# Performance work log

Hardware: AMD Instinct MI355X
Metric: run time of the kernel (lower is better)

Reference implementation:

```python
import jax, jax.numpy as jnp
import numpy as np


def cosine_noise_schedule(t):
    # legacy mode: 1 - cos(t/1.008 * pi/2)^2
    return 1.0 - jnp.cos(t / 1.008 * jnp.pi / 2.0) ** 2


def setup_inputs() -> dict:
    key = jax.random.key(0)
    k1, k2, k3 = jax.random.split(key, 3)
    x = jax.random.normal(k1, (256, 3, 32, 32), dtype=jnp.float32)
    images = jax.random.normal(k2, (50000, 3, 32, 32), dtype=jnp.float32)
    t = jax.random.uniform(k3, (1,), dtype=jnp.float32)
    return {"t": t, "x": x, "images": images}


def reference(t, x, images):
    # Exact ideal score: softmax over dataset of Gaussian kernel weights.
    # The original streams dataset batches with an online-softmax running max;
    # with uniform batch sizes that is mathematically a global softmax over N:
    #   score = -(x - at * E_p[y]) / bt^2,  p_j = softmax(-||x - at*y_j||^2 / (2 bt^2))
    sched = cosine_noise_schedule(t)          # [1]
    bt = jnp.sqrt(sched)                      # [1]
    at = jnp.sqrt(1.0 - sched)                # [1]
    b, c, h, w = x.shape
    n = images.shape[0]
    xf = x.reshape(b, -1)                     # [b, chw]
    yf = images.reshape(n, -1)                # [n, chw]
    # ||x - at*y||^2 = ||x||^2 + at^2 ||y||^2 - 2 at x.y  (GEMM-dominant)
    x2 = jnp.sum(xf * xf, axis=1)             # [b]
    y2 = jnp.sum(yf * yf, axis=1)             # [n]
    cross = xf @ yf.T                         # [b, n]
    d2 = x2[:, None] + (at ** 2) * y2[None, :] - 2.0 * at * cross  # [b, n]
    logits = -d2 / (2.0 * bt ** 2)            # [b, n]
    p = jax.nn.softmax(logits, axis=1)        # [b, n], stable (max-subtracted)
    ybar = (p @ yf).reshape(b, c, h, w)       # softmax-weighted dataset mean
    return -(x - at * ybar) / (bt ** 2)
```

## Files before the change

### kernel.cpp

```cpp
#include <hip/hip_runtime.h>

typedef float    f32x4  __attribute__((ext_vector_type(4)));
typedef float    f32x16 __attribute__((ext_vector_type(16)));
typedef _Float16 f16x4  __attribute__((ext_vector_type(4)));
typedef _Float16 f16x8  __attribute__((ext_vector_type(8)));

#define N_IMG 50000
#define NPAD  50176
#define BROWS 256
#define CHW   3072
#define BK    64
#define BM    128
#define BN    128
#define EHS   50176
#define KCHUNK 3136
#define NSPLIT 16

__device__ __forceinline__ void glds16(const void* g, void* l) {
    __builtin_amdgcn_global_load_lds(
        (const __attribute__((address_space(1))) void*)g,
        (__attribute__((address_space(3))) void*)l, 16, 0, 0);
}

__global__ void k_scalars(const float* __restrict__ t, float* __restrict__ sc) {
    if (threadIdx.x == 0) {
        double tv  = (double)t[0];
        double ang = tv * (1.5707963267948966 / 1.008);
        double c   = cos(ang);
        double at  = c;
        double bt2 = 1.0 - c * c;
        sc[0] = (float)at;
        sc[1] = (float)bt2;
        sc[2] = (float)(at / bt2);
        sc[3] = (float)(at * at * 0.5 / bt2);
        sc[4] = (float)(1.0 / bt2);
    }
}

__global__ void k_xprep(const float* __restrict__ x, _Float16* __restrict__ xh) {
    int idx = blockIdx.x * 256 + threadIdx.x;
    f32x4 v = ((const f32x4*)x)[idx];
    f16x4 h;
    h[0] = (_Float16)v[0]; h[1] = (_Float16)v[1];
    h[2] = (_Float16)v[2]; h[3] = (_Float16)v[3];
    ((f16x4*)xh)[idx] = h;
}

__global__ void k_prep(const float* __restrict__ img, _Float16* __restrict__ imgh,
                       float* __restrict__ y2) {
    int row = blockIdx.x, tid = threadIdx.x;
    f16x4* dst = (f16x4*)(imgh + (size_t)row * CHW);
    if (row >= N_IMG) {
        f16x4 z = {(_Float16)0.f, (_Float16)0.f, (_Float16)0.f, (_Float16)0.f};
        #pragma unroll
        for (int i = 0; i < 3; i++) dst[tid + i * 256] = z;
        return;
    }
    const f32x4* src = (const f32x4*)(img + (size_t)row * CHW);
    float s = 0.f;
    #pragma unroll
    for (int i = 0; i < 3; i++) {
        f32x4 v = src[tid + i * 256];
        s += v[0]*v[0] + v[1]*v[1] + v[2]*v[2] + v[3]*v[3];
        f16x4 h;
        h[0] = (_Float16)v[0]; h[1] = (_Float16)v[1];
        h[2] = (_Float16)v[2]; h[3] = (_Float16)v[3];
        dst[tid + i * 256] = h;
    }
    for (int o = 32; o > 0; o >>= 1) s += __shfl_down(s, o);
    __shared__ float wsum[4];
    if ((tid & 63) == 0) wsum[tid >> 6] = s;
    __syncthreads();
    if (tid == 0) y2[row] = (wsum[0] + wsum[1]) + (wsum[2] + wsum[3]);
}

__global__ __launch_bounds__(256, 3) void k_gemm1(
        const _Float16* __restrict__ xh, const _Float16* __restrict__ imgh,
        const float* __restrict__ y2g, const float* __restrict__ sc,
        float* __restrict__ logits) {
    __shared__ _Float16 Alds[BM * BK];
    __shared__ _Float16 Blds[BN * BK];

    const int tid = threadIdx.x;
    const int wid = tid >> 6, lane = tid & 63;
    const int flat = blockIdx.x;
    const int xcd = flat & 7, loc = flat >> 3;
    const int m0 = (loc & 1) * BM;
    const int n0 = (xcd * 49 + (loc >> 1)) * BN;

    const _Float16* gA[4]; const _Float16* gB[4];
    _Float16* lA[4]; _Float16* lB[4];
    #pragma unroll
    for (int j = 0; j < 4; j++) {
        int seg = wid * 4 + j;
        int row = seg * 8 + (lane >> 3);
        int off = (((lane & 7) ^ (row & 7)) << 3);
        gA[j] = xh + (size_t)(m0 + row) * CHW + off;
        int rb = n0 + row; if (rb > N_IMG - 1) rb = N_IMG - 1;
        gB[j] = imgh + (size_t)rb * CHW + off;
        lA[j] = Alds + seg * 512;
        lB[j] = Blds + seg * 512;
    }

    const int wm = wid >> 1, wn = wid & 1;
    const int rm = wm * 64, cn = wn * 64;
    const int lr = lane & 31, hi = lane >> 5;
    const int xm = (lr & 7) << 4;
    const char* Ab = (const char*)Alds;
    const char* Bb = (const char*)Blds;
    const int ar0 = (rm + lr) * 128,      ar1 = (rm + 32 + lr) * 128;
    const int br0 = (cn + lr) * 128,      br1 = (cn + 32 + lr) * 128;
    const int kof = hi * 16;

    f32x16 acc[2][2];
    #pragma unroll
    for (int mi = 0; mi < 2; mi++)
        #pragma unroll
        for (int ni = 0; ni < 2; ni++)
            #pragma unroll
            for (int r = 0; r < 16; r++) acc[mi][ni][r] = 0.f;

    for (int it = 0; it < CHW / BK; ++it) {
        if (it) __syncthreads();
        #pragma unroll
        for (int j = 0; j < 4; j++) glds16(gA[j] + it * BK, lA[j]);
        #pragma unroll
        for (int j = 0; j < 4; j++) glds16(gB[j] + it * BK, lB[j]);
        __syncthreads();
        #pragma unroll
        for (int ks = 0; ks < 4; ++ks) {
            int off = (ks * 32 + kof) ^ xm;
            f16x8 a0 = *(const f16x8*)(Ab + ar0 + off);
            f16x8 a1 = *(const f16x8*)(Ab + ar1 + off);
            f16x8 b0 = *(const f16x8*)(Bb + br0 + off);
            f16x8 b1 = *(const f16x8*)(Bb + br1 + off);
            acc[0][0] = __builtin_amdgcn_mfma_f32_32x32x16_f16(a0, b0, acc[0][0], 0, 0, 0);
            acc[0][1] = __builtin_amdgcn_mfma_f32_32x32x16_f16(a0, b1, acc[0][1], 0, 0, 0);
            acc[1][0] = __builtin_amdgcn_mfma_f32_32x32x16_f16(a1, b0, acc[1][0], 0, 0, 0);
            acc[1][1] = __builtin_amdgcn_mfma_f32_32x32x16_f16(a1, b1, acc[1][1], 0, 0, 0);
        }
    }

    const float c_cross = sc[2], c_y2 = sc[3];
    #pragma unroll
    for (int mi = 0; mi < 2; mi++)
        #pragma unroll
        for (int ni = 0; ni < 2; ni++) {
            int col = n0 + cn + ni * 32 + lr;
            if (col >= N_IMG) continue;
            float y2v = y2g[col];
            f32x16 v = acc[mi][ni];
            #pragma unroll
            for (int r = 0; r < 16; r++) {
                int row = m0 + rm + mi * 32 + (r & 3) + 8 * (r >> 2) + 4 * hi;
                logits[(size_t)row * N_IMG + col] = c_cross * v[r] - c_y2 * y2v;
            }
        }
}

__global__ void k_softmax(const float* __restrict__ logits, _Float16* __restrict__ eh,
                          float* __restrict__ rowsum) {
    int row = blockIdx.x, tid = threadIdx.x;
    const f32x4* lr = (const f32x4*)(logits + (size_t)row * N_IMG);
    _Float16* erow = eh + (size_t)row * EHS;
    f16x4* er = (f16x4*)erow;
    __shared__ float wred[4];

    if (tid < EHS - N_IMG) erow[N_IMG + tid] = (_Float16)0.f;

    float m = -3.0e38f;
    for (int i = tid; i < N_IMG / 4; i += 256) {
        f32x4 v = lr[i];
        m = fmaxf(m, fmaxf(fmaxf(v[0], v[1]), fmaxf(v[2], v[3])));
    }
    for (int o = 32; o > 0; o >>= 1) m = fmaxf(m, __shfl_down(m, o));
    if ((tid & 63) == 0) wred[tid >> 6] = m;
    __syncthreads();
    m = fmaxf(fmaxf(wred[0], wred[1]), fmaxf(wred[2], wred[3]));
    __syncthreads();

    float s = 0.f;
    for (int i = tid; i < N_IMG / 4; i += 256) {
        f32x4 v = lr[i];
        float e0 = __expf(v[0] - m), e1 = __expf(v[1] - m);
        float e2 = __expf(v[2] - m), e3 = __expf(v[3] - m);
        s += (e0 + e1) + (e2 + e3);
        f16x4 h;
        h[0] = (_Float16)e0; h[1] = (_Float16)e1;
        h[2] = (_Float16)e2; h[3] = (_Float16)e3;
        er[i] = h;
    }
    for (int o = 32; o > 0; o >>= 1) s += __shfl_down(s, o);
    if ((tid & 63) == 0) wred[tid >> 6] = s;
    __syncthreads();
    if (tid == 0) rowsum[row] = (wred[0] + wred[1]) + (wred[2] + wred[3]);
}

__global__ __launch_bounds__(256, 3) void k_gemm2(
        const _Float16* __restrict__ eh, const _Float16* __restrict__ imgh,
        float* __restrict__ partial) {
    __shared__ _Float16 Alds[BM * BK];
    __shared__ _Float16 Blds[BN * BK];
    __shared__ _Float16 Tmp[BK * BN];

    const int tid = threadIdx.x;
    const int wid = tid >> 6, lane = tid & 63;
    const int flat = blockIdx.x;
    const int xcd = flat & 7, loc = flat >> 3;
    const int ck  = xcd * 2 + (loc >= 48 ? 1 : 0);
    const int rem = loc - (loc >= 48 ? 48 : 0);
    const int m0 = (rem & 1) * BM;
    const int d0 = (rem >> 1) * BN;
    const int kbase = ck * KCHUNK;

    const _Float16* gA[4]; _Float16* lA[4];
    const _Float16* gB[4]; _Float16* lB[4];
    #pragma unroll
    for (int j = 0; j < 4; j++) {
        int seg = wid * 4 + j;
        int row = seg * 8 + (lane >> 3);
        int off = (((lane & 7) ^ (row & 7)) << 3);
        gA[j] = eh + (size_t)(m0 + row) * EHS + kbase + off;
        lA[j] = Alds + seg * 512;
        gB[j] = imgh + (size_t)(kbase + seg * 4 + (lane >> 4)) * CHW + d0 + (lane & 15) * 8;
        lB[j] = Tmp + seg * 512;
    }

    const int q   = tid & 31;
    const int oct = tid >> 5;

    const int wm = wid >> 1, wn = wid & 1;
    const int rm = wm * 64, cn = wn * 64;
    const int lr = lane & 31, hi = lane >> 5;
    const int xm = (lr & 7) << 4;
    const int ar0 = (rm + lr) * 128, ar1 = (rm + 32 + lr) * 128;
    const int br0 = (cn + lr) * 128, br1 = (cn + 32 + lr) * 128;
    const int kof = hi * 16;

    f32x16 acc[2][2];
    #pragma unroll
    for (int mi = 0; mi < 2; mi++)
        #pragma unroll
        for (int ni = 0; ni < 2; ni++)
            #pragma unroll
            for (int r = 0; r < 16; r++) acc[mi][ni][r] = 0.f;

    for (int it = 0; it < KCHUNK / BK; ++it) {
        __syncthreads();
        #pragma unroll
        for (int j = 0; j < 4; j++) glds16(gA[j] + it * BK, lA[j]);
        #pragma unroll
        for (int j = 0; j < 4; j++) glds16(gB[j] + (size_t)it * BK * CHW, lB[j]);
        __syncthreads();

        {
            f16x4 r[8];
            #pragma unroll
            for (int j = 0; j < 8; j++)
                r[j] = *(const f16x4*)&Tmp[(oct * 8 + j) * 128 + q * 4];
            #pragma unroll
            for (int dd = 0; dd < 4; dd++) {
                f16x8 w;
                #pragma unroll
                for (int j = 0; j < 8; j++) w[j] = r[j][dd];
                int d = q * 4 + dd;
                *(f16x8*)((char*)Blds + d * 128 + ((oct ^ (d & 7)) << 4)) = w;
            }
        }
        __syncthreads();

        const char* Ab = (const char*)Alds;
        const char* Bb = (const char*)Blds;
        #pragma unroll
        for (int ks = 0; ks < 4; ++ks) {
            int off = (ks * 32 + kof) ^ xm;
            f16x8 a0 = *(const f16x8*)(Ab + ar0 + off);
            f16x8 a1 = *(const f16x8*)(Ab + ar1 + off);
            f16x8 b0 = *(const f16x8*)(Bb + br0 + off);
            f16x8 b1 = *(const f16x8*)(Bb + br1 + off);
            acc[0][0] = __builtin_amdgcn_mfma_f32_32x32x16_f16(a0, b0, acc[0][0], 0, 0, 0);
            acc[0][1] = __builtin_amdgcn_mfma_f32_32x32x16_f16(a0, b1, acc[0][1], 0, 0, 0);
            acc[1][0] = __builtin_amdgcn_mfma_f32_32x32x16_f16(a1, b0, acc[1][0], 0, 0, 0);
            acc[1][1] = __builtin_amdgcn_mfma_f32_32x32x16_f16(a1, b1, acc[1][1], 0, 0, 0);
        }
    }

    float* pp = partial + (size_t)ck * BROWS * CHW;
    #pragma unroll
    for (int mi = 0; mi < 2; mi++)
        #pragma unroll
        for (int ni = 0; ni < 2; ni++) {
            int dcol = d0 + cn + ni * 32 + lr;
            f32x16 v = acc[mi][ni];
            #pragma unroll
            for (int r = 0; r < 16; r++) {
                int row = m0 + rm + mi * 32 + (r & 3) + 8 * (r >> 2) + 4 * hi;
                pp[(size_t)row * CHW + dcol] = v[r];
            }
        }
}

__global__ void k_final(const float* __restrict__ partial, const float* __restrict__ x,
                        const float* __restrict__ rowsum, const float* __restrict__ sc,
                        float* __restrict__ out) {
    int idx = blockIdx.x * 256 + threadIdx.x;
    int row = idx / (CHW / 4);
    float at = sc[0], invbt2 = sc[4];
    float scale = at * invbt2 / rowsum[row];
    const f32x4* p4 = (const f32x4*)partial;
    f32x4 s = p4[idx];
    #pragma unroll
    for (int c = 1; c < NSPLIT; c++) s = s + p4[(size_t)c * (BROWS * CHW / 4) + idx];
    f32x4 xv = ((const f32x4*)x)[idx];
    f32x4 o;
    #pragma unroll
    for (int j = 0; j < 4; j++) o[j] = s[j] * scale - xv[j] * invbt2;
    ((f32x4*)out)[idx] = o;
}

extern "C" void kernel_launch(void* const* d_in, const int* in_sizes, int n_in,
                              void* d_out, int out_size, void* d_ws, size_t ws_size,
                              hipStream_t stream) {
    const float* t   = (const float*)d_in[0];
    const float* x   = (const float*)d_in[1];
    const float* img = (const float*)d_in[2];
    float* out = (float*)d_out;
    char* ws = (char*)d_ws;

    float*    sc     = (float*)(ws + 0);
    float*    rowsum = (float*)(ws + 256);
    float*    y2     = (float*)(ws + 4096);
    _Float16* xh     = (_Float16*)(ws + 212992);
    _Float16* imgh   = (_Float16*)(ws + 2097152);
    _Float16* eh     = (_Float16*)(ws + 310378496);
    float*    logits = (float*)(ws + 336068608);
    float*    partial = logits;

    k_scalars<<<1, 64, 0, stream>>>(t, sc);
    k_xprep<<<(BROWS * CHW / 4) / 256, 256, 0, stream>>>(x, xh);
    k_prep<<<NPAD, 256, 0, stream>>>(img, imgh, y2);
    k_gemm1<<<784, 256, 0, stream>>>(xh, imgh, y2, sc, logits);
    k_softmax<<<256, 256, 0, stream>>>(logits, eh, rowsum);
    k_gemm2<<<768, 256, 0, stream>>>(eh, imgh, partial);
    k_final<<<(BROWS * CHW / 4) / 256, 256, 0, stream>>>(partial, x, rowsum, sc, out);
}
```

Baseline: 481.5 us.

## Prefetch next K-tile into LDS while computing current MFMA tile

Restructures the p@Y GEMM main loop so the next iteration's global-to-LDS loads are issued before the MFMA work of the current tile. The A fragments are read into registers before the barrier, which frees the A buffer and the staging buffer for the next tile. Overlapping global latency with compute removes one barrier per iteration. The cost is extra register pressure from holding the A fragments, and a reliance on correct waitcnt handling for the async LDS loads.

```diff
diff --git a/kernel.cpp b/kernel.cpp
--- a/kernel.cpp
+++ b/kernel.cpp
@@ -236,6 +236,8 @@
     const int ar0 = (rm + lr) * 128, ar1 = (rm + 32 + lr) * 128;
     const int br0 = (cn + lr) * 128, br1 = (cn + 32 + lr) * 128;
     const int kof = hi * 16;
+    const char* Ab = (const char*)Alds;
+    const char* Bb = (const char*)Blds;
 
     f32x16 acc[2][2];
     #pragma unroll
@@ -244,15 +246,23 @@
         for (int ni = 0; ni < 2; ni++)
             #pragma unroll
             for (int r = 0; r < 16; r++) acc[mi][ni][r] = 0.f;
+
+    #pragma unroll
+    for (int j = 0; j < 4; j++) glds16(gA[j], lA[j]);
+    #pragma unroll
+    for (int j = 0; j < 4; j++) glds16(gB[j], lB[j]);
+
+    f16x8 afr0[4], afr1[4];
 
     for (int it = 0; it < KCHUNK / BK; ++it) {
         __syncthreads();
-        #pragma unroll
-        for (int j = 0; j < 4; j++) glds16(gA[j] + it * BK, lA[j]);
-        #pragma unroll
-        for (int j = 0; j < 4; j++) glds16(gB[j] + (size_t)it * BK * CHW, lB[j]);
-        __syncthreads();
-
+
+        #pragma unroll
+        for (int ks = 0; ks < 4; ++ks) {
+            int offa = (ks * 32 + kof) ^ xm;
+            afr0[ks] = *(const f16x8*)(Ab + ar0 + offa);
+            afr1[ks] = *(const f16x8*)(Ab + ar1 + offa);
+        }
         {
             f16x4 r[8];
             #pragma unroll
@@ -269,19 +279,21 @@
         }
         __syncthreads();
 
-        const char* Ab = (const char*)Alds;
-        const char* Bb = (const char*)Blds;
+        if (it + 1 < KCHUNK / BK) {
+            #pragma unroll
+            for (int j = 0; j < 4; j++) glds16(gA[j] + (it + 1) * BK, lA[j]);
+            #pragma unroll
+            for (int j = 0; j < 4; j++) glds16(gB[j] + (size_t)(it + 1) * BK * CHW, lB[j]);
+        }
         #pragma unroll
         for (int ks = 0; ks < 4; ++ks) {
-            int off = (ks * 32 + kof) ^ xm;
-            f16x8 a0 = *(const f16x8*)(Ab + ar0 + off);
-            f16x8 a1 = *(const f16x8*)(Ab + ar1 + off);
-            f16x8 b0 = *(const f16x8*)(Bb + br0 + off);
-            f16x8 b1 = *(const f16x8*)(Bb + br1 + off);
-            acc[0][0] = __builtin_amdgcn_mfma_f32_32x32x16_f16(a0, b0, acc[0][0], 0, 0, 0);
-            acc[0][1] = __builtin_amdgcn_mfma_f32_32x32x16_f16(a0, b1, acc[0][1], 0, 0, 0);
-            acc[1][0] = __builtin_amdgcn_mfma_f32_32x32x16_f16(a1, b0, acc[1][0], 0, 0, 0);
-            acc[1][1] = __builtin_amdgcn_mfma_f32_32x32x16_f16(a1, b1, acc[1][1], 0, 0, 0);
+            int offb = (ks * 32 + kof) ^ xm;
+            f16x8 b0 = *(const f16x8*)(Bb + br0 + offb);
+            f16x8 b1 = *(const f16x8*)(Bb + br1 + offb);
+            acc[0][0] = __builtin_amdgcn_mfma_f32_32x32x16_f16(afr0[ks], b0, acc[0][0], 0, 0, 0);
+            acc[0][1] = __builtin_amdgcn_mfma_f32_32x32x16_f16(afr0[ks], b1, acc[0][1], 0, 0, 0);
+            acc[1][0] = __builtin_amdgcn_mfma_f32_32x32x16_f16(afr1[ks], b0, acc[1][0], 0, 0, 0);
+            acc[1][1] = __builtin_amdgcn_mfma_f32_32x32x16_f16(afr1[ks], b1, acc[1][1], 0, 0, 0);
         }
     }
 
```

New measurement: 481.2 us. Within noise of the previous version (-0.1%).
